# Kernel optimization log

Measured on AMD Instinct MI355X. Metric: run time of the kernel, lower is better.

The kernel has to match this reference:

```python
import jax, jax.numpy as jnp
import numpy as np

THRESHOLD = 0.05
STRIDE = (1, 1)
PADDING = ((1, 1), (1, 1))


def ternary_quantize(w, threshold=THRESHOLD):
    # w -> {-1, 0, +1}; zero where |w| <= threshold
    mask = (jnp.abs(w) > threshold).astype(w.dtype)
    return jnp.sign(w) * mask


def setup_inputs() -> dict:
    key = jax.random.key(0)
    k1, k2 = jax.random.split(key)
    B, Cin, H, W = 32, 256, 56, 56
    Cout, kH, kW = 256, 3, 3
    fan_in = Cin * kH * kW
    std = np.sqrt(2.0 / fan_in) * 2.0
    x = jax.random.normal(k1, (B, Cin, H, W), dtype=jnp.float32)
    weight = jax.random.normal(k2, (Cout, Cin, kH, kW), dtype=jnp.float32) * std
    bias = jnp.zeros((Cout,), dtype=jnp.float32)
    return {"x": x, "weight": weight, "bias": bias}


def reference(x, weight, bias):
    w_t = ternary_quantize(weight, THRESHOLD)
    out = jax.lax.conv_general_dilated(
        x, w_t,
        window_strides=STRIDE,
        padding=PADDING,
        dimension_numbers=("NCHW", "OIHW", "NCHW"),
    )
    return out + bias[None, :, None, None]
```

## Files before the change

kernel.cpp:

```cpp
#include <hip/hip_runtime.h>

#define CIN   256
#define COUT  256
#define HH    56
#define WW    56
#define BATCH 32
#define KTOT  2304
#define HP    58
#define WP    58
#define NPIX  (BATCH*HH*WW)
#define HWSZ  (HH*WW)
#define KT    36

typedef __bf16 bf16x8 __attribute__((ext_vector_type(8)));
typedef float  f32x4  __attribute__((ext_vector_type(4)));

#define AS1 __attribute__((address_space(1)))
#define AS3 __attribute__((address_space(3)))

__device__ __forceinline__ unsigned short f2bf(float f) {
  union { float f; unsigned int u; } v; v.f = f;
  unsigned int u = v.u;
  u += 0x7fffu + ((u >> 16) & 1u);
  return (unsigned short)(u >> 16);
}

__device__ __forceinline__ void async16(const void* g, void* l) {
  __builtin_amdgcn_global_load_lds((const AS1 unsigned int*)g,
                                   (AS3 unsigned int*)l, 16, 0, 0);
}

__global__ __launch_bounds__(256) void quant_w(const float* __restrict__ w,
                                               unsigned short* __restrict__ wr) {
  int tid = blockIdx.x * 256 + threadIdx.x;
  if (tid >= COUT * KTOT) return;
  int co  = tid / KTOT;
  int rem = tid - co * KTOT;
  int tap = rem >> 8;
  int ci  = rem & 255;
  int kh  = tap / 3;
  int kw  = tap - kh * 3;
  float v = w[((co * CIN + ci) * 3 + kh) * 3 + kw];
  float q = (fabsf(v) > 0.05f) ? ((v > 0.f) ? 1.f : -1.f) : 0.f;
  wr[tid] = f2bf(q);
}

#define TSTR 60
__global__ __launch_bounds__(256) void pad_nhwc(const float* __restrict__ x,
                                                unsigned short* __restrict__ xp) {
  const int nhp = blockIdx.x;
  const int n   = nhp / HP;
  const int hp  = nhp - n * HP;
  const int ci0 = blockIdx.y * 64;
  const int t   = threadIdx.x;
  const size_t obase = (size_t)nhp * (WP * 256);

  __shared__ __align__(16) float tile[64 * TSTR];
  const bool hborder = (hp == 0) || (hp == HP - 1);

  if (!hborder) {
    const int h = hp - 1;
    #pragma unroll
    for (int it = 0; it < 4; ++it) {
      int linear = it * 256 + t;
      if (linear < 896) {
        int cil = linear / 14;
        int w4  = linear - cil * 14;
        *(float4*)&tile[cil * TSTR + w4 * 4] =
            *(const float4*)&x[(((size_t)(n * CIN + ci0 + cil)) * HH + h) * WW + w4 * 4];
      }
    }
  }
  __syncthreads();

  #pragma unroll
  for (int it = 0; it < 2; ++it) {
    int linear = it * 256 + t;
    if (linear < 464) {
      int wp = linear >> 3;
      int g  = linear & 7;
      unsigned int pk[4] = {0u, 0u, 0u, 0u};
      if (!hborder && wp != 0 && wp != WP - 1) {
        #pragma unroll
        for (int j = 0; j < 4; ++j) {
          unsigned int lo = f2bf(tile[(g * 8 + 2 * j) * TSTR + (wp - 1)]);
          unsigned int hi = f2bf(tile[(g * 8 + 2 * j + 1) * TSTR + (wp - 1)]);
          pk[j] = lo | (hi << 16);
        }
      }
      uint4 v; v.x = pk[0]; v.y = pk[1]; v.z = pk[2]; v.w = pk[3];
      *(uint4*)(xp + obase + (size_t)wp * 256 + ci0 + g * 8) = v;
    }
  }
}


__device__ __forceinline__ int xko_of(int kk) {
  int tap = kk >> 2;
  int k3  = tap / 3;
  int w3  = tap - k3 * 3;
  return (k3 * WP + w3) * 256 + ((kk & 3) << 6);
}

#define NOWAIT (void)0
#define VM8 asm volatile("s_waitcnt vmcnt(8)" ::: "memory")
#define VM4 asm volatile("s_waitcnt vmcnt(4)" ::: "memory")
#define VM0 asm volatile("s_waitcnt vmcnt(0)" ::: "memory")

#define STAGE_A(b_, kh_, kkq_) do {                                           \
  const size_t ko_ = (size_t)(kkq_) * 64 + (kh_) * 32;                        \
  char* d_ = smem + (((b_) * 2 + (kh_)) * 16384) + t * 16;                    \
  async16(Wr + aOff0 + ko_, d_);                                              \
  async16(Wr + aOff1 + ko_, d_ + 8192);                                       \
} while (0)

#define STAGE_B(b_, kh_, xko_) do {                                           \
  const size_t ko_ = (size_t)(xko_) + (kh_) * 32;                             \
  char* d_ = smem + 65536 + (((b_) * 2 + (kh_)) * 16384) + t * 16;            \
  async16(Xp + bOff0 + ko_, d_);                                              \
  async16(Xp + bOff1 + ko_, d_ + 8192);                                       \
} while (0)

#define PHASE(b_, kh_, mh_, WAITE, ...) do {                                  \
  const int abase_ = ((b_) * 2 + (kh_)) * 16384;                              \
  const int bbase_ = 65536 + ((b_) * 2 + (kh_)) * 16384;                      \
  bf16x8 af_[4];                                                              \
  _Pragma("unroll")                                                           \
  for (int mt = 0; mt < 4; ++mt)                                              \
    af_[mt] = *(const bf16x8*)(smem + abase_ + rdA + (mh_) * 4096 + mt * 1024);\
  if ((mh_) == 0) {                                                           \
    _Pragma("unroll")                                                         \
    for (int nt = 0; nt < 4; ++nt)                                            \
      bfr[nt] = *(const bf16x8*)(smem + bbase_ + rdB + nt * 1024);            \
  }                                                                           \
  __VA_ARGS__;                                                                \
  __builtin_amdgcn_s_barrier();                                               \
  asm volatile("s_waitcnt lgkmcnt(0)" ::: "memory");                          \
  __builtin_amdgcn_sched_barrier(0);                                          \
  __builtin_amdgcn_s_setprio(1);                                              \
  _Pragma("unroll")                                                           \
  for (int mt = 0; mt < 4; ++mt)                                              \
    _Pragma("unroll")                                                         \
    for (int nt = 0; nt < 4; ++nt)                                            \
      acc[(mh_) * 4 + mt][nt] = __builtin_amdgcn_mfma_f32_16x16x32_bf16(      \
          af_[mt], bfr[nt], acc[(mh_) * 4 + mt][nt], 0, 0, 0);                \
  __builtin_amdgcn_s_setprio(0);                                              \
  WAITE;                                                                      \
  __builtin_amdgcn_s_barrier();                                               \
} while (0)

#define TILE_FULL(b_, kk_) do {                                               \
  const int kkn1_ = (kk_) + 1, kkn2_ = (kk_) + 2;                             \
  const int xko1_ = xko_of(kkn1_), xko2_ = xko_of(kkn2_);                     \
  PHASE(b_, 0, 0, NOWAIT, STAGE_A((b_) ^ 1, 1, kkn1_));                       \
  PHASE(b_, 0, 1, VM8,    STAGE_B((b_) ^ 1, 1, xko1_));                       \
  PHASE(b_, 1, 0, NOWAIT, STAGE_A((b_), 0, kkn2_));                           \
  PHASE(b_, 1, 1, VM8,    STAGE_B((b_), 0, xko2_));                           \
} while (0)

__global__ __launch_bounds__(512, 2) void conv_gemm(
    const unsigned short* __restrict__ Wr,
    const unsigned short* __restrict__ Xp,
    const float* __restrict__ bias,
    float* __restrict__ out) {
  extern __shared__ char smem[];

  const int t    = threadIdx.x;
  const int lane = t & 63;
  const int wv   = t >> 6;
  const int wm   = wv >> 2;
  const int wn   = wv & 3;
  const int l15  = lane & 15;
  const int quad = lane >> 4;

  const int bid = blockIdx.x;
  const int pb  = (bid & 7) * 49 + (bid >> 3);
  const int p0  = pb * 256;

  const int srow = t >> 2;
  const int schk = (t & 3) ^ ((srow >> 1) & 3);
  const size_t aOff0 = (size_t)srow * KTOT + schk * 8;
  const size_t aOff1 = aOff0 + (size_t)128 * KTOT;

  const int pA = p0 + srow;
  const int pB = pA + 128;
  const int nA = pA / HWSZ;  const int hwA = pA - nA * HWSZ;
  const int hA = hwA / WW;   const int wA  = hwA - hA * WW;
  const int nB = pB / HWSZ;  const int hwB = pB - nB * HWSZ;
  const int hB = hwB / WW;   const int wB  = hwB - hB * WW;
  const size_t bOff0 = ((size_t)((nA * HP + hA) * WP + wA)) * 256 + schk * 8;
  const size_t bOff1 = ((size_t)((nB * HP + hB) * WP + wB)) * 256 + schk * 8;

  const int rchk = ((quad ^ ((l15 >> 1) & 3)) * 16);
  const int rdA  = (wm * 128 + l15) * 64 + rchk;
  const int rdB  = (wn * 64 + l15) * 64 + rchk;

  f32x4 acc[8][4];
  #pragma unroll
  for (int i = 0; i < 8; ++i)
    #pragma unroll
    for (int j = 0; j < 4; ++j)
      acc[i][j] = (f32x4){0.f, 0.f, 0.f, 0.f};
  bf16x8 bfr[4];

  STAGE_A(0, 0, 0);
  STAGE_B(0, 0, xko_of(0));
  STAGE_A(0, 1, 0);
  STAGE_B(0, 1, xko_of(0));
  STAGE_A(1, 0, 1);
  STAGE_B(1, 0, xko_of(1));
  VM8;
  __builtin_amdgcn_s_barrier();

  #pragma unroll 1
  for (int kk = 0; kk < 34; kk += 2) {
    TILE_FULL(0, kk);
    TILE_FULL(1, kk + 1);
  }
  {
    const int xko35 = xko_of(35);
    PHASE(0, 0, 0, NOWAIT, STAGE_A(1, 1, 35));
    PHASE(0, 0, 1, VM8,    STAGE_B(1, 1, xko35));
    PHASE(0, 1, 0, NOWAIT, NOWAIT);
    PHASE(0, 1, 1, VM4,    NOWAIT);
  }
  {
    PHASE(1, 0, 0, NOWAIT, NOWAIT);
    PHASE(1, 0, 1, VM0,    NOWAIT);
    PHASE(1, 1, 0, NOWAIT, NOWAIT);
    PHASE(1, 1, 1, NOWAIT, NOWAIT);
  }

  float bv[8][4];
  #pragma unroll
  for (int m = 0; m < 8; ++m)
    #pragma unroll
    for (int r = 0; r < 4; ++r)
      bv[m][r] = bias[wm * 128 + m * 16 + quad * 4 + r];

  #pragma unroll
  for (int nt = 0; nt < 4; ++nt) {
    const int p  = p0 + wn * 64 + nt * 16 + l15;
    const int np = p / HWSZ;
    const int hw = p - np * HWSZ;
    const size_t obase = (size_t)np * (COUT * HWSZ) + hw;
    #pragma unroll
    for (int m = 0; m < 8; ++m) {
      const int co = wm * 128 + m * 16 + quad * 4;
      #pragma unroll
      for (int r = 0; r < 4; ++r)
        out[obase + (size_t)(co + r) * HWSZ] = acc[m][nt][r] + bv[m][r];
    }
  }
}

extern "C" void kernel_launch(void* const* d_in, const int* in_sizes, int n_in,
                              void* d_out, int out_size, void* d_ws, size_t ws_size,
                              hipStream_t stream) {
  const float* x    = (const float*)d_in[0];
  const float* w    = (const float*)d_in[1];
  const float* bias = (const float*)d_in[2];
  float* out        = (float*)d_out;

  unsigned short* xp = (unsigned short*)d_ws;
  unsigned short* wr = (unsigned short*)((char*)d_ws + 55115776);

  quant_w<<<dim3((COUT * KTOT) / 256), dim3(256), 0, stream>>>(w, wr);
  pad_nhwc<<<dim3(BATCH * HP, 4), dim3(256), 0, stream>>>(x, xp);

  (void)hipFuncSetAttribute((const void*)conv_gemm,
                            hipFuncAttributeMaxDynamicSharedMemorySize, 131072);
  conv_gemm<<<dim3(392), dim3(512), 131072, stream>>>(wr, xp, bias, out);
}
```

Baseline: 327.0 us.

## Restructure LDS staging into full-K64 double buffer with 8-chunk XOR swizzle

Replaces the half-tile (K=32) staged pipeline, whose loads were interleaved across phases with partial vmcnt waits, by a simple double buffer of full 64-wide K tiles. Each tile uses 128-byte rows with an 8-way XOR swizzle. Loads for the next K step are issued across the first three phases and drained with vmcnt(0) at the end of each step. The aim is simpler addressing, fewer barriers per tile and wider rows per lane. The cost is a shorter prefetch distance, since there is one full wait per iteration, which may expose global-load latency.

```diff
diff --git a/kernel.cpp b/kernel.cpp
--- a/kernel.cpp
+++ b/kernel.cpp
@@ -95,45 +95,25 @@
 }
 
 
-__device__ __forceinline__ int xko_of(int kk) {
-  int tap = kk >> 2;
-  int k3  = tap / 3;
-  int w3  = tap - k3 * 3;
-  return (k3 * WP + w3) * 256 + ((kk & 3) << 6);
-}
-
 #define NOWAIT (void)0
-#define VM8 asm volatile("s_waitcnt vmcnt(8)" ::: "memory")
-#define VM4 asm volatile("s_waitcnt vmcnt(4)" ::: "memory")
 #define VM0 asm volatile("s_waitcnt vmcnt(0)" ::: "memory")
 
-#define STAGE_A(b_, kh_, kkq_) do {                                           \
-  const size_t ko_ = (size_t)(kkq_) * 64 + (kh_) * 32;                        \
-  char* d_ = smem + (((b_) * 2 + (kh_)) * 16384) + t * 16;                    \
-  async16(Wr + aOff0 + ko_, d_);                                              \
-  async16(Wr + aOff1 + ko_, d_ + 8192);                                       \
-} while (0)
-
-#define STAGE_B(b_, kh_, xko_) do {                                           \
-  const size_t ko_ = (size_t)(xko_) + (kh_) * 32;                             \
-  char* d_ = smem + 65536 + (((b_) * 2 + (kh_)) * 16384) + t * 16;            \
-  async16(Xp + bOff0 + ko_, d_);                                              \
-  async16(Xp + bOff1 + ko_, d_ + 8192);                                       \
-} while (0)
-
-#define PHASE(b_, kh_, mh_, WAITE, ...) do {                                  \
-  const int abase_ = ((b_) * 2 + (kh_)) * 16384;                              \
-  const int bbase_ = 65536 + ((b_) * 2 + (kh_)) * 16384;                      \
+#define SA(bn_, s_) async16(Wr + koW + aSrc##s_, smem + (bn_) + (s_)*8192 + t*16)
+#define SB(bn_, s_) async16(Xp + koX + bSrc[s_], smem + 65536 + (bn_) + (s_)*8192 + t*16)
+
+#define PHASE(ab_, kq_, mh_, WAITE, ...) do {                                 \
+  __VA_ARGS__;                                                                \
   bf16x8 af_[4];                                                              \
   _Pragma("unroll")                                                           \
   for (int mt = 0; mt < 4; ++mt)                                              \
-    af_[mt] = *(const bf16x8*)(smem + abase_ + rdA + (mh_) * 4096 + mt * 1024);\
+    af_[mt] = *(const bf16x8*)(smem + (ab_) + rA + (mh_)*8192 + mt*2048 +     \
+                               ((kq_) ? cX1 : cX0));                          \
   if ((mh_) == 0) {                                                           \
     _Pragma("unroll")                                                         \
     for (int nt = 0; nt < 4; ++nt)                                            \
-      bfr[nt] = *(const bf16x8*)(smem + bbase_ + rdB + nt * 1024);            \
+      bfr[nt] = *(const bf16x8*)(smem + 65536 + (ab_) + rB + nt*2048 +        \
+                                 ((kq_) ? cX1 : cX0));                        \
   }                                                                           \
-  __VA_ARGS__;                                                                \
   __builtin_amdgcn_s_barrier();                                               \
   asm volatile("s_waitcnt lgkmcnt(0)" ::: "memory");                          \
   __builtin_amdgcn_sched_barrier(0);                                          \
@@ -142,20 +122,11 @@
   for (int mt = 0; mt < 4; ++mt)                                              \
     _Pragma("unroll")                                                         \
     for (int nt = 0; nt < 4; ++nt)                                            \
-      acc[(mh_) * 4 + mt][nt] = __builtin_amdgcn_mfma_f32_16x16x32_bf16(      \
-          af_[mt], bfr[nt], acc[(mh_) * 4 + mt][nt], 0, 0, 0);                \
+      acc[(mh_)*4+mt][nt] = __builtin_amdgcn_mfma_f32_16x16x32_bf16(          \
+          af_[mt], bfr[nt], acc[(mh_)*4+mt][nt], 0, 0, 0);                    \
   __builtin_amdgcn_s_setprio(0);                                              \
   WAITE;                                                                      \
   __builtin_amdgcn_s_barrier();                                               \
-} while (0)
-
-#define TILE_FULL(b_, kk_) do {                                               \
-  const int kkn1_ = (kk_) + 1, kkn2_ = (kk_) + 2;                             \
-  const int xko1_ = xko_of(kkn1_), xko2_ = xko_of(kkn2_);                     \
-  PHASE(b_, 0, 0, NOWAIT, STAGE_A((b_) ^ 1, 1, kkn1_));                       \
-  PHASE(b_, 0, 1, VM8,    STAGE_B((b_) ^ 1, 1, xko1_));                       \
-  PHASE(b_, 1, 0, NOWAIT, STAGE_A((b_), 0, kkn2_));                           \
-  PHASE(b_, 1, 1, VM8,    STAGE_B((b_), 0, xko2_));                           \
 } while (0)
 
 __global__ __launch_bounds__(512, 2) void conv_gemm(
@@ -177,23 +148,27 @@
   const int pb  = (bid & 7) * 49 + (bid >> 3);
   const int p0  = pb * 256;
 
-  const int srow = t >> 2;
-  const int schk = (t & 3) ^ ((srow >> 1) & 3);
-  const size_t aOff0 = (size_t)srow * KTOT + schk * 8;
-  const size_t aOff1 = aOff0 + (size_t)128 * KTOT;
-
-  const int pA = p0 + srow;
-  const int pB = pA + 128;
-  const int nA = pA / HWSZ;  const int hwA = pA - nA * HWSZ;
-  const int hA = hwA / WW;   const int wA  = hwA - hA * WW;
-  const int nB = pB / HWSZ;  const int hwB = pB - nB * HWSZ;
-  const int hB = hwB / WW;   const int wB  = hwB - hB * WW;
-  const size_t bOff0 = ((size_t)((nA * HP + hA) * WP + wA)) * 256 + schk * 8;
-  const size_t bOff1 = ((size_t)((nB * HP + hB) * WP + wB)) * 256 + schk * 8;
-
-  const int rchk = ((quad ^ ((l15 >> 1) & 3)) * 16);
-  const int rdA  = (wm * 128 + l15) * 64 + rchk;
-  const int rdB  = (wn * 64 + l15) * 64 + rchk;
+  const int srow  = t >> 3;
+  const int sclog = (t & 7) ^ (srow & 7);
+
+  const size_t aSrc0 = (size_t)srow * KTOT + sclog * 8;
+  const size_t aSrc1 = aSrc0 + (size_t)64  * KTOT;
+  const size_t aSrc2 = aSrc0 + (size_t)128 * KTOT;
+  const size_t aSrc3 = aSrc0 + (size_t)192 * KTOT;
+
+  size_t bSrc[4];
+  #pragma unroll
+  for (int s = 0; s < 4; ++s) {
+    int p = p0 + s * 64 + srow;
+    int n = p / HWSZ; int hw = p - n * HWSZ;
+    int h = hw / WW;  int w = hw - h * WW;
+    bSrc[s] = ((size_t)((n * HP + h) * WP + w)) * 256 + sclog * 8;
+  }
+
+  const int rA  = (wm * 128 + l15) * 128;
+  const int rB  = (wn * 64  + l15) * 128;
+  const int cX0 = ((quad      ^ (lane & 7)) * 16);
+  const int cX1 = (((4 + quad) ^ (lane & 7)) * 16);
 
   f32x4 acc[8][4];
   #pragma unroll
@@ -203,32 +178,36 @@
       acc[i][j] = (f32x4){0.f, 0.f, 0.f, 0.f};
   bf16x8 bfr[4];
 
-  STAGE_A(0, 0, 0);
-  STAGE_B(0, 0, xko_of(0));
-  STAGE_A(0, 1, 0);
-  STAGE_B(0, 1, xko_of(0));
-  STAGE_A(1, 0, 1);
-  STAGE_B(1, 0, xko_of(1));
-  VM8;
+  {
+    const size_t koW = 0;
+    const size_t koX = 0;
+    SA(0, 0); SA(0, 1); SA(0, 2); SA(0, 3);
+    SB(0, 0); SB(0, 1); SB(0, 2); SB(0, 3);
+  }
+  VM0;
   __builtin_amdgcn_s_barrier();
 
   #pragma unroll 1
-  for (int kk = 0; kk < 34; kk += 2) {
-    TILE_FULL(0, kk);
-    TILE_FULL(1, kk + 1);
+  for (int kk = 0; kk < 35; ++kk) {
+    const int ab = (kk & 1) << 15;
+    const int bn = 32768 - ab;
+    const int kn = kk + 1;
+    const size_t koW = (size_t)kn * 64;
+    const int tapn = kn >> 2;
+    const int khn  = tapn / 3;
+    const int kwn  = tapn - khn * 3;
+    const size_t koX = (size_t)((khn * WP + kwn) * 256 + ((kn & 3) << 6));
+
+    PHASE(ab, 0, 0, NOWAIT, SA(bn, 0); SA(bn, 1); SA(bn, 2));
+    PHASE(ab, 0, 1, NOWAIT, SA(bn, 3); SB(bn, 0); SB(bn, 1));
+    PHASE(ab, 1, 0, NOWAIT, SB(bn, 2); SB(bn, 3));
+    PHASE(ab, 1, 1, VM0,    NOWAIT);
   }
   {
-    const int xko35 = xko_of(35);
-    PHASE(0, 0, 0, NOWAIT, STAGE_A(1, 1, 35));
-    PHASE(0, 0, 1, VM8,    STAGE_B(1, 1, xko35));
-    PHASE(0, 1, 0, NOWAIT, NOWAIT);
-    PHASE(0, 1, 1, VM4,    NOWAIT);
-  }
-  {
-    PHASE(1, 0, 0, NOWAIT, NOWAIT);
-    PHASE(1, 0, 1, VM0,    NOWAIT);
-    PHASE(1, 1, 0, NOWAIT, NOWAIT);
-    PHASE(1, 1, 1, NOWAIT, NOWAIT);
+    PHASE(32768, 0, 0, NOWAIT, NOWAIT);
+    PHASE(32768, 0, 1, NOWAIT, NOWAIT);
+    PHASE(32768, 1, 0, NOWAIT, NOWAIT);
+    PHASE(32768, 1, 1, NOWAIT, NOWAIT);
   }
 
   float bv[8][4];
```

Measured after the change: 335.3 us. +2.5%, slower.
